# Performance work log

Hardware: AMD Instinct MI355X
Metric: run time of the kernel (lower is better)

Reference implementation:

```python
import jax, jax.numpy as jnp
import numpy as np

N_HEADS = 16

def setup_inputs() -> dict:
    key = jax.random.key(0)
    k1, k2 = jax.random.split(key)
    qkv = jax.random.normal(k1, (2, 3072, 2048), dtype=jnp.float32)
    encoder_kv = jax.random.normal(k2, (2, 2048, 512), dtype=jnp.float32)
    return {"qkv": qkv, "encoder_kv": encoder_kv}

def reference(qkv, encoder_kv):
    bs, width, length = qkv.shape
    ch = width // (3 * N_HEADS)  # 64
    # [bs*H, 3*ch, T] -> q, k, v each [bs*H, ch, T]
    qkv_r = qkv.reshape(bs * N_HEADS, ch * 3, length)
    q, k, v = qkv_r[:, :ch], qkv_r[:, ch:2 * ch], qkv_r[:, 2 * ch:]
    # encoder kv: [bs*H, 2*ch, S] -> ek, ev; prepend to k/v along token axis
    ekv = encoder_kv.reshape(bs * N_HEADS, ch * 2, -1)
    ek, ev = ekv[:, :ch], ekv[:, ch:]
    k = jnp.concatenate([ek, k], axis=-1)  # [bs*H, ch, S+T]
    v = jnp.concatenate([ev, v], axis=-1)
    scale = 1.0 / (ch ** 0.25)  # split pre-scaling as in original
    weight = jnp.einsum('bct,bcs->bts', q * scale, k * scale)  # [bs*H, T, S+T]
    weight = jax.nn.softmax(weight.astype(jnp.float32), axis=-1).astype(weight.dtype)
    a = jnp.einsum('bts,bcs->bct', weight, v)  # [bs*H, ch, T]
    return a.reshape(bs, -1, length)
```

## Files before the change

### kernel.cpp

```cpp
#include <hip/hip_runtime.h>


#define QT_BYTES (32u * 2048u * 128u)
#define KV_TILE  16384
#define N_ST     40

typedef _Float16 h4 __attribute__((ext_vector_type(4)));
typedef _Float16 h8 __attribute__((ext_vector_type(8)));
typedef __fp16   g2 __attribute__((ext_vector_type(2)));
typedef float    f4 __attribute__((ext_vector_type(4)));

typedef __attribute__((address_space(1))) const unsigned int GAS;
typedef __attribute__((address_space(3))) unsigned int LAS;

static __device__ __forceinline__ void dma16(const void* g, void* l) {
    __builtin_amdgcn_global_load_lds((GAS*)g, (LAS*)l, 16, 0, 0);
}

static __device__ __forceinline__ unsigned short f2h(float f) {
    union { _Float16 h; unsigned short u; } v;
    v.h = (_Float16)f;
    return v.u;
}

__global__ __launch_bounds__(256) void prep_kernel(
        const float* __restrict__ qkv,
        const float* __restrict__ ekv,
        char* __restrict__ ws) {
    __shared__ __align__(16) unsigned short sT[64 * 80];
    const int tid = threadIdx.x;
    const int tile = blockIdx.x;

    if (tile < 2304) {
        const float* src; int stride; char* dst; float scale;
        if (tile < 1024) {
            int bh = tile >> 5, tt = tile & 31;
            int b = bh >> 4, h = bh & 15;
            src = qkv + (size_t)b * 6291456 + (size_t)(h * 192) * 2048 + tt * 64;
            stride = 2048;
            dst = ws + (size_t)bh * 262144 + (size_t)tt * 8192;
            scale = 0.18033688f;
        } else {
            int i = tile - 1024; int bh = i / 40, st = i - bh * 40;
            int b = bh >> 4, h = bh & 15;
            if (st < 8) { src = ekv + (size_t)b * 1048576 + (size_t)(h * 128) * 512 + st * 64; stride = 512; }
            else        { src = qkv + (size_t)b * 6291456 + (size_t)(h * 192 + 64) * 2048 + (size_t)(st - 8) * 64; stride = 2048; }
            dst = ws + QT_BYTES + ((size_t)bh * 40 + st) * KV_TILE;
            scale = 1.0f;
        }
        const int c = tid >> 2, t4 = (tid & 3) * 16;
        #pragma unroll
        for (int i = 0; i < 4; ++i) {
            int t = t4 + i * 4;
            float4 v = *(const float4*)(src + (size_t)c * stride + t);
            sT[(t + 0) * 80 + c] = f2h(v.x * scale);
            sT[(t + 1) * 80 + c] = f2h(v.y * scale);
            sT[(t + 2) * 80 + c] = f2h(v.z * scale);
            sT[(t + 3) * 80 + c] = f2h(v.w * scale);
        }
        __syncthreads();
        #pragma unroll
        for (int ii = 0; ii < 2; ++ii) {
            int idx = tid * 2 + ii;
            int r = idx >> 3, pc = idx & 7;
            int lc = pc ^ (r & 7);
            *(uint4*)(dst + r * 128 + pc * 16) = *(const uint4*)(sT + r * 80 + lc * 8);
        }
    } else {
        int i = tile - 2304; int bh = i / 40, st = i - bh * 40;
        int b = bh >> 4, h = bh & 15;
        const float* src; int stride;
        if (st < 8) { src = ekv + (size_t)b * 1048576 + (size_t)(h * 128 + 64) * 512 + st * 64; stride = 512; }
        else        { src = qkv + (size_t)b * 6291456 + (size_t)(h * 192 + 128) * 2048 + (size_t)(st - 8) * 64; stride = 2048; }
        char* dst = ws + QT_BYTES + ((size_t)bh * 40 + st) * KV_TILE + 8192;
        const int c = tid >> 2, s16 = (tid & 3) * 16;
        #pragma unroll
        for (int g = 0; g < 2; ++g) {
            float4 a  = *(const float4*)(src + (size_t)c * stride + s16 + g * 8);
            float4 bb = *(const float4*)(src + (size_t)c * stride + s16 + g * 8 + 4);
            unsigned int u0 = (unsigned int)f2h(a.x)  | ((unsigned int)f2h(a.y)  << 16);
            unsigned int u1 = (unsigned int)f2h(a.z)  | ((unsigned int)f2h(a.w)  << 16);
            unsigned int u2 = (unsigned int)f2h(bb.x) | ((unsigned int)f2h(bb.y) << 16);
            unsigned int u3 = (unsigned int)f2h(bb.z) | ((unsigned int)f2h(bb.w) << 16);
            int pc = ((s16 >> 3) + g) ^ (c & 7);
            uint4 pk = {u0, u1, u2, u3};
            *(uint4*)(dst + c * 128 + pc * 16) = pk;
        }
    }
}

__global__ __launch_bounds__(512, 4) void attn_fwd(
        const char* __restrict__ ws,
        float* __restrict__ out) {
    __shared__ __align__(16) char smem[65536];

    const int tid = threadIdx.x;
    const int w = tid >> 6, lane = tid & 63;
    const int pair = w >> 1;
    const int par  = w & 1;
    const int sub  = w >> 1;
    const int quad = lane >> 4, nn = lane & 15;

    const int lid = blockIdx.x;
    const int bh = (lid & 7) * 4 + (lid >> 7);
    const int t0 = ((lid >> 3) & 15) * 128;
    const int b = bh >> 4, h = bh & 15;

    const char* qsrc  = ws + (size_t)bh * 262144 + (size_t)t0 * 128;
    const char* kvsrc = ws + QT_BYTES + (size_t)bh * 40 * KV_TILE;

    #pragma unroll
    for (int i = 0; i < 4; ++i) {
        int off = (sub * 4 + i) * 1024;
        dma16(kvsrc + (size_t)par * KV_TILE + off + lane * 16,
              smem + par * 16384 + off);
    }

    h8 qb[2][2];
    #pragma unroll
    for (int nt = 0; nt < 2; ++nt) {
        int r = pair * 32 + nt * 16 + nn;
        #pragma unroll
        for (int kh = 0; kh < 2; ++kh)
            qb[nt][kh] = __builtin_nontemporal_load(
                (const h8*)(qsrc + r * 128 + (((kh * 4 + quad) ^ (nn & 7)) * 16)));
    }
    __syncthreads();

    f4 o[2][4];
    f4 lacc[2];
    #pragma unroll
    for (int nt = 0; nt < 2; ++nt) {
        lacc[nt][0] = 0.f; lacc[nt][1] = 0.f; lacc[nt][2] = 0.f; lacc[nt][3] = 0.f;
        #pragma unroll
        for (int cm = 0; cm < 4; ++cm) {
            o[nt][cm][0] = 0.f; o[nt][cm][1] = 0.f; o[nt][cm][2] = 0.f; o[nt][cm][3] = 0.f;
        }
    }
    const h4 ones4 = {(_Float16)1.f, (_Float16)1.f, (_Float16)1.f, (_Float16)1.f};
    const int sw = nn & 7;

    for (int it = 0; it < N_ST / 2; ++it) {
        char* cur = smem + ((it & 1) * 2 + par) * 16384;
        if (it < N_ST / 2 - 1) {
            char* nxt = smem + ((((it + 1) & 1) * 2) + par) * 16384;
            const char* g = kvsrc + (size_t)(2 * (it + 1) + par) * KV_TILE;
            #pragma unroll
            for (int i = 0; i < 4; ++i) {
                int off = (sub * 4 + i) * 1024;
                dma16(g + off + lane * 16, nxt + off);
            }
        }
        const char* sK = cur;
        const char* sV = cur + 8192;

        #pragma unroll
        for (int ct = 0; ct < 4; ++ct) {
            h8 ka0 = *(const h8*)(sK + (ct * 16 + nn) * 128 + ((quad ^ sw) * 16));
            h8 ka1 = *(const h8*)(sK + (ct * 16 + nn) * 128 + (((4 + quad) ^ sw) * 16));
            h4 va[4];
            {
                int lc = 2 * ct + (quad >> 1);
                int vo = ((lc ^ sw) * 16) + (quad & 1) * 8;
                #pragma unroll
                for (int cm = 0; cm < 4; ++cm)
                    va[cm] = *(const h4*)(sV + (cm * 16 + nn) * 128 + vo);
            }
            __builtin_amdgcn_s_setprio(1);
            #pragma unroll
            for (int nt = 0; nt < 2; ++nt) {
                f4 z = {0.f, 0.f, 0.f, 0.f};
                z = __builtin_amdgcn_mfma_f32_16x16x32_f16(ka0, qb[nt][0], z, 0, 0, 0);
                z = __builtin_amdgcn_mfma_f32_16x16x32_f16(ka1, qb[nt][1], z, 0, 0, 0);
                float e0 = __builtin_amdgcn_exp2f(z[0]);
                float e1 = __builtin_amdgcn_exp2f(z[1]);
                float e2 = __builtin_amdgcn_exp2f(z[2]);
                float e3 = __builtin_amdgcn_exp2f(z[3]);
                union { g2 g[2]; h4 h; } pu;
                pu.g[0] = __builtin_amdgcn_cvt_pkrtz(e0, e1);
                pu.g[1] = __builtin_amdgcn_cvt_pkrtz(e2, e3);
                h4 pb = pu.h;
                lacc[nt] = __builtin_amdgcn_mfma_f32_16x16x16f16(ones4, pb, lacc[nt], 0, 0, 0);
                #pragma unroll
                for (int cm = 0; cm < 4; ++cm)
                    o[nt][cm] = __builtin_amdgcn_mfma_f32_16x16x16f16(va[cm], pb, o[nt][cm], 0, 0, 0);
            }
            __builtin_amdgcn_s_setprio(0);
        }
        __syncthreads();
    }

    char* scr = smem + pair * 10240;
    if (par == 1) {
        #pragma unroll
        for (int nt = 0; nt < 2; ++nt) {
            #pragma unroll
            for (int cm = 0; cm < 4; ++cm)
                *(f4*)(scr + (nt * 4 + cm) * 1024 + lane * 16) = o[nt][cm];
            *(float*)(scr + 8192 + nt * 256 + lane * 4) = lacc[nt][0];
        }
    }
    __syncthreads();
    if (par == 0) {
        float* outp = out + (size_t)b * 2097152 + (size_t)(h * 64) * 2048 + t0;
        #pragma unroll
        for (int nt = 0; nt < 2; ++nt) {
            float pl = *(const float*)(scr + 8192 + nt * 256 + lane * 4);
            float rl = 1.0f / (lacc[nt][0] + pl);
            int t = pair * 32 + nt * 16 + nn;
            #pragma unroll
            for (int cm = 0; cm < 4; ++cm) {
                f4 po = *(const f4*)(scr + (nt * 4 + cm) * 1024 + lane * 16);
                #pragma unroll
                for (int r2 = 0; r2 < 4; ++r2) {
                    int c = cm * 16 + quad * 4 + r2;
                    __builtin_nontemporal_store((o[nt][cm][r2] + po[r2]) * rl,
                                                outp + (size_t)c * 2048 + t);
                }
            }
        }
    }
}

extern "C" void kernel_launch(void* const* d_in, const int* in_sizes, int n_in,
                              void* d_out, int out_size, void* d_ws, size_t ws_size,
                              hipStream_t stream) {
    const float* qkv = (const float*)d_in[0];
    const float* ekv = (const float*)d_in[1];
    float* out = (float*)d_out;
    char* ws = (char*)d_ws;

    prep_kernel<<<3584, 256, 0, stream>>>(qkv, ekv, ws);
    attn_fwd<<<512, 512, 0, stream>>>(ws, out);
}
```

Baseline: 144.5 us.

## Split each KV tile across four waves and halve query tile per block

The attention kernel now processes 64 query rows per block instead of 128, launching 1024 blocks. Each KV tile is split four ways across waves, with 2 query groups of 16 rows each, instead of two ways. LDS drops from 64 KiB to 34 KiB and launch bounds allow 8 waves per SIMD, aiming at higher occupancy and better CU fill. The cost is a two-stage cross-wave reduction of partial outputs through LDS with extra barriers, and twice as many KV tile loads per query row.

```diff
diff --git a/kernel.cpp b/kernel.cpp
--- a/kernel.cpp
+++ b/kernel.cpp
@@ -89,31 +89,29 @@
     }
 }
 
-__global__ __launch_bounds__(512, 4) void attn_fwd(
+__global__ __launch_bounds__(512, 8) void attn_fwd(
         const char* __restrict__ ws,
         float* __restrict__ out) {
-    __shared__ __align__(16) char smem[65536];
+    __shared__ __align__(16) char smem[34816];
 
     const int tid = threadIdx.x;
     const int w = tid >> 6, lane = tid & 63;
-    const int pair = w >> 1;
-    const int par  = w & 1;
-    const int sub  = w >> 1;
+    const int pair = w >> 2;
+    const int spar = w & 3;
     const int quad = lane >> 4, nn = lane & 15;
 
     const int lid = blockIdx.x;
-    const int bh = (lid & 7) * 4 + (lid >> 7);
-    const int t0 = ((lid >> 3) & 15) * 128;
+    const int bh = (lid & 7) * 4 + (lid >> 8);
+    const int t0 = ((lid >> 3) & 31) * 64;
     const int b = bh >> 4, h = bh & 15;
 
     const char* qsrc  = ws + (size_t)bh * 262144 + (size_t)t0 * 128;
     const char* kvsrc = ws + QT_BYTES + (size_t)bh * 40 * KV_TILE;
 
     #pragma unroll
-    for (int i = 0; i < 4; ++i) {
-        int off = (sub * 4 + i) * 1024;
-        dma16(kvsrc + (size_t)par * KV_TILE + off + lane * 16,
-              smem + par * 16384 + off);
+    for (int i = 0; i < 2; ++i) {
+        int off = w * 2048 + i * 1024;
+        dma16(kvsrc + off + lane * 16, smem + off);
     }
 
     h8 qb[2][2];
@@ -140,58 +138,54 @@
     const h4 ones4 = {(_Float16)1.f, (_Float16)1.f, (_Float16)1.f, (_Float16)1.f};
     const int sw = nn & 7;
 
-    for (int it = 0; it < N_ST / 2; ++it) {
-        char* cur = smem + ((it & 1) * 2 + par) * 16384;
-        if (it < N_ST / 2 - 1) {
-            char* nxt = smem + ((((it + 1) & 1) * 2) + par) * 16384;
-            const char* g = kvsrc + (size_t)(2 * (it + 1) + par) * KV_TILE;
-            #pragma unroll
-            for (int i = 0; i < 4; ++i) {
-                int off = (sub * 4 + i) * 1024;
+    for (int it = 0; it < N_ST; ++it) {
+        const char* cur = smem + (it & 1) * 16384;
+        if (it < N_ST - 1) {
+            char* nxt = smem + ((it + 1) & 1) * 16384;
+            const char* g = kvsrc + (size_t)(it + 1) * KV_TILE;
+            #pragma unroll
+            for (int i = 0; i < 2; ++i) {
+                int off = w * 2048 + i * 1024;
                 dma16(g + off + lane * 16, nxt + off);
             }
         }
         const char* sK = cur;
         const char* sV = cur + 8192;
 
-        #pragma unroll
-        for (int ct = 0; ct < 4; ++ct) {
-            h8 ka0 = *(const h8*)(sK + (ct * 16 + nn) * 128 + ((quad ^ sw) * 16));
-            h8 ka1 = *(const h8*)(sK + (ct * 16 + nn) * 128 + (((4 + quad) ^ sw) * 16));
-            h4 va[4];
-            {
-                int lc = 2 * ct + (quad >> 1);
-                int vo = ((lc ^ sw) * 16) + (quad & 1) * 8;
-                #pragma unroll
-                for (int cm = 0; cm < 4; ++cm)
-                    va[cm] = *(const h4*)(sV + (cm * 16 + nn) * 128 + vo);
-            }
-            __builtin_amdgcn_s_setprio(1);
-            #pragma unroll
-            for (int nt = 0; nt < 2; ++nt) {
-                f4 z = {0.f, 0.f, 0.f, 0.f};
-                z = __builtin_amdgcn_mfma_f32_16x16x32_f16(ka0, qb[nt][0], z, 0, 0, 0);
-                z = __builtin_amdgcn_mfma_f32_16x16x32_f16(ka1, qb[nt][1], z, 0, 0, 0);
-                float e0 = __builtin_amdgcn_exp2f(z[0]);
-                float e1 = __builtin_amdgcn_exp2f(z[1]);
-                float e2 = __builtin_amdgcn_exp2f(z[2]);
-                float e3 = __builtin_amdgcn_exp2f(z[3]);
-                union { g2 g[2]; h4 h; } pu;
-                pu.g[0] = __builtin_amdgcn_cvt_pkrtz(e0, e1);
-                pu.g[1] = __builtin_amdgcn_cvt_pkrtz(e2, e3);
-                h4 pb = pu.h;
-                lacc[nt] = __builtin_amdgcn_mfma_f32_16x16x16f16(ones4, pb, lacc[nt], 0, 0, 0);
-                #pragma unroll
-                for (int cm = 0; cm < 4; ++cm)
-                    o[nt][cm] = __builtin_amdgcn_mfma_f32_16x16x16f16(va[cm], pb, o[nt][cm], 0, 0, 0);
-            }
-            __builtin_amdgcn_s_setprio(0);
+        const int srow = spar * 16 + nn;
+        h8 ka0 = *(const h8*)(sK + srow * 128 + ((quad ^ sw) * 16));
+        h8 ka1 = *(const h8*)(sK + srow * 128 + (((4 + quad) ^ sw) * 16));
+        h4 va[4];
+        {
+            int lc = 2 * spar + (quad >> 1);
+            int vo = ((lc ^ sw) * 16) + (quad & 1) * 8;
+            #pragma unroll
+            for (int cm = 0; cm < 4; ++cm)
+                va[cm] = *(const h4*)(sV + (cm * 16 + nn) * 128 + vo);
+        }
+        #pragma unroll
+        for (int nt = 0; nt < 2; ++nt) {
+            f4 z = {0.f, 0.f, 0.f, 0.f};
+            z = __builtin_amdgcn_mfma_f32_16x16x32_f16(ka0, qb[nt][0], z, 0, 0, 0);
+            z = __builtin_amdgcn_mfma_f32_16x16x32_f16(ka1, qb[nt][1], z, 0, 0, 0);
+            float e0 = __builtin_amdgcn_exp2f(z[0]);
+            float e1 = __builtin_amdgcn_exp2f(z[1]);
+            float e2 = __builtin_amdgcn_exp2f(z[2]);
+            float e3 = __builtin_amdgcn_exp2f(z[3]);
+            union { g2 g[2]; h4 h; } pu;
+            pu.g[0] = __builtin_amdgcn_cvt_pkrtz(e0, e1);
+            pu.g[1] = __builtin_amdgcn_cvt_pkrtz(e2, e3);
+            h4 pb = pu.h;
+            lacc[nt] = __builtin_amdgcn_mfma_f32_16x16x16f16(ones4, pb, lacc[nt], 0, 0, 0);
+            #pragma unroll
+            for (int cm = 0; cm < 4; ++cm)
+                o[nt][cm] = __builtin_amdgcn_mfma_f32_16x16x16f16(va[cm], pb, o[nt][cm], 0, 0, 0);
         }
         __syncthreads();
     }
 
-    char* scr = smem + pair * 10240;
-    if (par == 1) {
+    if (spar >= 2) {
+        char* scr = smem + (pair * 2 + (spar - 2)) * 8704;
         #pragma unroll
         for (int nt = 0; nt < 2; ++nt) {
             #pragma unroll
@@ -201,7 +195,30 @@
         }
     }
     __syncthreads();
-    if (par == 0) {
+    if (spar < 2) {
+        const char* scr = smem + (pair * 2 + spar) * 8704;
+        #pragma unroll
+        for (int nt = 0; nt < 2; ++nt) {
+            #pragma unroll
+            for (int cm = 0; cm < 4; ++cm)
+                o[nt][cm] = o[nt][cm] + *(const f4*)(scr + (nt * 4 + cm) * 1024 + lane * 16);
+            lacc[nt][0] += *(const float*)(scr + 8192 + nt * 256 + lane * 4);
+        }
+    }
+    __syncthreads();
+    if (spar == 1) {
+        char* scr = smem + pair * 8704;
+        #pragma unroll
+        for (int nt = 0; nt < 2; ++nt) {
+            #pragma unroll
+            for (int cm = 0; cm < 4; ++cm)
+                *(f4*)(scr + (nt * 4 + cm) * 1024 + lane * 16) = o[nt][cm];
+            *(float*)(scr + 8192 + nt * 256 + lane * 4) = lacc[nt][0];
+        }
+    }
+    __syncthreads();
+    if (spar == 0) {
+        const char* scr = smem + pair * 8704;
         float* outp = out + (size_t)b * 2097152 + (size_t)(h * 64) * 2048 + t0;
         #pragma unroll
         for (int nt = 0; nt < 2; ++nt) {
@@ -231,5 +248,5 @@
     char* ws = (char*)d_ws;
 
     prep_kernel<<<3584, 256, 0, stream>>>(qkv, ekv, ws);
-    attn_fwd<<<512, 512, 0, stream>>>(ws, out);
-}
+    attn_fwd<<<1024, 512, 0, stream>>>(ws, out);
+}
```

After: 390.9 us. 170% more time.
